# Performance work log

Measured on AMD Instinct MI355X. Metric: run time of the kernel, lower is better.

Reference implementation:

```python
import jax, jax.numpy as jnp
import numpy as np


def setup_inputs() -> dict:
    key = jax.random.key(0)
    k1, k2, k3, k4 = jax.random.split(key, 4)
    B, T, D, U = 64, 2048, 256, 256
    X = jax.random.normal(k1, (B, T, D), dtype=jnp.float32)
    # scale weights ~ Glorot-ish so activations stay in range
    kernel = jax.random.normal(k2, (D, 3 * U), dtype=jnp.float32) / np.sqrt(D)
    recurrent_kernel = jax.random.normal(k3, (U, 3 * U), dtype=jnp.float32) / np.sqrt(U)
    bias = jax.random.normal(k4, (3 * U,), dtype=jnp.float32) * 0.01
    return {"X": X, "kernel": kernel, "recurrent_kernel": recurrent_kernel, "bias": bias}


def reference(X, kernel, recurrent_kernel, bias):
    # X: [B, T, D]; kernel: [D, 3U]; recurrent_kernel: [U, 3U]; bias: [3U]
    U = recurrent_kernel.shape[0]
    B = X.shape[0]
    Uz = recurrent_kernel[:, :U]
    Ur = recurrent_kernel[:, U:2 * U]
    Uh = recurrent_kernel[:, 2 * U:]
    # Precompute input projections for all timesteps in one GEMM (same math
    # as per-step matmul(x, W*) + B*).
    proj = X @ kernel + bias            # [B, T, 3U]
    proj = jnp.swapaxes(proj, 0, 1)     # [T, B, 3U] for scan over time
    xz = proj[:, :, :U]
    xr = proj[:, :, U:2 * U]
    xh = proj[:, :, 2 * U:]

    def step(a, xs):
        tz, tr, th = xs                  # each [B, U]
        z = jax.nn.sigmoid(a @ Uz + tz)
        r = jax.nn.sigmoid(a @ Ur + tr)
        h = jnp.tanh((r * a) @ Uh + th)
        a = z * a + (1.0 - z) * h
        return a, None

    a0 = jnp.zeros((B, U), dtype=X.dtype)
    a_final, _ = jax.lax.scan(step, a0, (xz, xr, xh))
    return a_final  # [B, U]
```

## Files before the change

### kernel.cpp

```cpp
#include <hip/hip_runtime.h>


typedef _Float16 half2_t __attribute__((ext_vector_type(2)));
typedef _Float16 half8_t __attribute__((ext_vector_type(8)));
typedef float    float4_t __attribute__((ext_vector_type(4)));

#define T_LEN 2048
#define B_SZ  64
#define D_IN  256
#define N3    768
#define U_SZ  256

#define H2(v, p) __builtin_shufflevector((v), (v), 2*(p), 2*(p)+1)

__device__ __forceinline__ float fdot2f(half2_t a, half2_t b, float c) {
#if __has_builtin(__builtin_amdgcn_fdot2)
    return __builtin_amdgcn_fdot2(a, b, c, false);
#else
    return c + (float)a[0]*(float)b[0] + (float)a[1]*(float)b[1];
#endif
}

__device__ __forceinline__ float fast_sigmoid(float s) {
    return __builtin_amdgcn_rcpf(1.0f + __builtin_amdgcn_exp2f(-1.44269504f * s));
}
__device__ __forceinline__ float fast_tanh(float s) {
    return 1.0f - 2.0f * __builtin_amdgcn_rcpf(1.0f + __builtin_amdgcn_exp2f(2.88539008f * s));
}

#define GA_LD 264
#define NT_N  16
#define MT_M  2048

__global__ __launch_bounds__(256) void proj_gemm(
    const float* __restrict__ X, const float* __restrict__ W,
    const float* __restrict__ bias, _Float16* __restrict__ proj)
{
    __shared__ __align__(16) _Float16 Ah[64 * GA_LD];
    __shared__ __align__(16) _Float16 Wh[48 * GA_LD];

    unsigned bid = blockIdx.x;
    unsigned idx = bid >> 3;
    unsigned mt  = (bid & 7) * (MT_M / 8) + (idx >> 4);
    unsigned nt  = idx & (NT_N - 1);
    int m0 = mt * 64, n0 = nt * 48;
    int tid = threadIdx.x;

    {
        int r = tid >> 6;
        int k = (tid & 63) * 4;
        #pragma unroll
        for (int i = 0; i < 16; ++i) {
            int row = i * 4 + r;
            float4_t v = *(const float4_t*)(X + (size_t)(m0 + row) * D_IN + k);
            _Float16* p = Ah + row * GA_LD + k;
            p[0] = (_Float16)v.x; p[1] = (_Float16)v.y;
            p[2] = (_Float16)v.z; p[3] = (_Float16)v.w;
        }
    }
    {
        int c  = tid & 63;
        int kk = tid >> 6;
        if (c < 48) {
            #pragma unroll 4
            for (int i = 0; i < 64; ++i) {
                int krow = i * 4 + kk;
                Wh[c * GA_LD + krow] = (_Float16)W[(size_t)krow * N3 + n0 + c];
            }
        }
    }
    __syncthreads();

    int r0 = (tid >> 4) << 2;
    int c  = tid & 15;
    float acc[4][3];
    #pragma unroll
    for (int rr = 0; rr < 4; ++rr)
        #pragma unroll
        for (int cc = 0; cc < 3; ++cc) acc[rr][cc] = 0.0f;

    for (int j = 0; j < 32; ++j) {
        half8_t av[4], wv[3];
        #pragma unroll
        for (int rr = 0; rr < 4; ++rr)
            av[rr] = *(const half8_t*)(Ah + (r0 + rr) * GA_LD + j * 8);
        #pragma unroll
        for (int cc = 0; cc < 3; ++cc)
            wv[cc] = *(const half8_t*)(Wh + (c + 16 * cc) * GA_LD + j * 8);
        #pragma unroll
        for (int rr = 0; rr < 4; ++rr)
            #pragma unroll
            for (int cc = 0; cc < 3; ++cc) {
                acc[rr][cc] = fdot2f(H2(av[rr],0), H2(wv[cc],0), acc[rr][cc]);
                acc[rr][cc] = fdot2f(H2(av[rr],1), H2(wv[cc],1), acc[rr][cc]);
                acc[rr][cc] = fdot2f(H2(av[rr],2), H2(wv[cc],2), acc[rr][cc]);
                acc[rr][cc] = fdot2f(H2(av[rr],3), H2(wv[cc],3), acc[rr][cc]);
            }
    }

    float bv[3];
    #pragma unroll
    for (int cc = 0; cc < 3; ++cc) bv[cc] = bias[n0 + c + 16 * cc];
    #pragma unroll
    for (int rr = 0; rr < 4; ++rr)
        #pragma unroll
        for (int cc = 0; cc < 3; ++cc)
            proj[(size_t)(m0 + r0 + rr) * N3 + (n0 + c + 16 * cc)] =
                (_Float16)(acc[rr][cc] + bv[cc]);
}

__global__ __launch_bounds__(512, 2) void gru_scan(
    const float* __restrict__ RK, const _Float16* __restrict__ proj,
    float* __restrict__ out)
{
    __shared__ __align__(16) _Float16 aH[U_SZ];
    __shared__ __align__(16) _Float16 raH[U_SZ];
    __shared__ float zS[U_SZ];
    __shared__ float aF[U_SZ];

    const int b    = blockIdx.x;
    const int tid  = threadIdx.x;
    const int g    = tid >> 8;
    const int u    = tid & 255;
    const int hcol = tid >> 1;
    const int kh   = tid & 1;

    half2_t wA[128];
    {
        const float* wp = RK + (size_t)(g << 8) + u;
        #pragma unroll
        for (int k2 = 0; k2 < 128; ++k2) {
            half2_t h;
            h[0] = (_Float16)wp[(size_t)(2 * k2)     * N3];
            h[1] = (_Float16)wp[(size_t)(2 * k2 + 1) * N3];
            wA[k2] = h;
        }
    }
    half2_t wB[64];
    {
        const float* wq = RK + (size_t)(kh * 128) * N3 + 512 + hcol;
        #pragma unroll
        for (int k2 = 0; k2 < 64; ++k2) {
            half2_t h;
            h[0] = (_Float16)wq[(size_t)(2 * k2)     * N3];
            h[1] = (_Float16)wq[(size_t)(2 * k2 + 1) * N3];
            wB[k2] = h;
        }
    }

    if (tid < U_SZ) { aF[tid] = 0.0f; aH[tid] = (_Float16)0.0f; }

    const _Float16* px1 = proj + ((size_t)b * T_LEN) * N3 + (g << 8) + u;
    const _Float16* px2 = proj + ((size_t)b * T_LEN) * N3 + 512 + hcol;
    float x1 = (float)px1[0];
    float x2 = (float)px2[0];
    __syncthreads();

    for (int t = 0; t < T_LEN; ++t) {
        const float x1c = x1, x2c = x2;
        if (t + 1 < T_LEN) {
            x1 = (float)px1[(size_t)(t + 1) * N3];
            x2 = (float)px2[(size_t)(t + 1) * N3];
        }

        {
            float a0 = 0.f, a1 = 0.f, a2 = 0.f, a3 = 0.f;
            #pragma unroll
            for (int j = 0; j < 32; ++j) {
                half8_t av = *(const half8_t*)(aH + j * 8);
                a0 = fdot2f(H2(av,0), wA[4*j+0], a0);
                a1 = fdot2f(H2(av,1), wA[4*j+1], a1);
                a2 = fdot2f(H2(av,2), wA[4*j+2], a2);
                a3 = fdot2f(H2(av,3), wA[4*j+3], a3);
            }
            float sig = fast_sigmoid((a0 + a1) + (a2 + a3) + x1c);
            if (g == 0) zS[u]  = sig;
            else        raH[u] = (_Float16)(sig * aF[u]);
        }
        __syncthreads();

        {
            float b0 = 0.f, b1 = 0.f, b2 = 0.f, b3 = 0.f;
            const _Float16* rbase = raH + (kh << 7);
            #pragma unroll
            for (int j = 0; j < 16; ++j) {
                half8_t rv = *(const half8_t*)(rbase + j * 8);
                b0 = fdot2f(H2(rv,0), wB[4*j+0], b0);
                b1 = fdot2f(H2(rv,1), wB[4*j+1], b1);
                b2 = fdot2f(H2(rv,2), wB[4*j+2], b2);
                b3 = fdot2f(H2(rv,3), wB[4*j+3], b3);
            }
            float hs = (b0 + b1) + (b2 + b3);
            hs += __shfl_xor(hs, 1, 64);
            if (kh == 0) {
                float h  = fast_tanh(hs + x2c);
                float z  = zS[hcol];
                float an = z * aF[hcol] + (1.0f - z) * h;
                aF[hcol] = an;
                aH[hcol] = (_Float16)an;
            }
        }
        __syncthreads();
    }

    if (tid < U_SZ) out[(size_t)b * U_SZ + tid] = aF[tid];
}

extern "C" void kernel_launch(void* const* d_in, const int* in_sizes, int n_in,
                              void* d_out, int out_size, void* d_ws, size_t ws_size,
                              hipStream_t stream)
{
    const float* X    = (const float*)d_in[0];
    const float* W    = (const float*)d_in[1];
    const float* RK   = (const float*)d_in[2];
    const float* bias = (const float*)d_in[3];
    _Float16* proj = (_Float16*)d_ws;

    proj_gemm<<<MT_M * NT_N, 256, 0, stream>>>(X, W, bias, proj);
    gru_scan<<<B_SZ, 512, 0, stream>>>(RK, proj, (float*)d_out);
}
```

Before: 3.717 ms.

## Split GRU scan dot products across 1024 threads with shuffle reductions

Doubles the scan block to 1024 threads, so each recurrent-gate column is split over two threads and each candidate column over four, with partial sums combined by warp shuffles. Each thread now does half as many dot-product steps per timestep, which shortens the serial critical path of the recurrence. The cost is extra shuffle and reduction steps, fewer threads doing useful nonlinear work, and a larger block to synchronise at each barrier. Per-thread register weight storage is halved.

```diff
diff --git a/kernel.cpp b/kernel.cpp
--- a/kernel.cpp
+++ b/kernel.cpp
@@ -109,7 +109,7 @@
                 (_Float16)(acc[rr][cc] + bv[cc]);
 }
 
-__global__ __launch_bounds__(512, 2) void gru_scan(
+__global__ __launch_bounds__(1024) void gru_scan(
     const float* __restrict__ RK, const _Float16* __restrict__ proj,
     float* __restrict__ out)
 {
@@ -120,27 +120,27 @@
 
     const int b    = blockIdx.x;
     const int tid  = threadIdx.x;
-    const int g    = tid >> 8;
-    const int u    = tid & 255;
-    const int hcol = tid >> 1;
-    const int kh   = tid & 1;
-
-    half2_t wA[128];
-    {
-        const float* wp = RK + (size_t)(g << 8) + u;
-        #pragma unroll
-        for (int k2 = 0; k2 < 128; ++k2) {
+    const int col1 = tid >> 1;
+    const int kh1  = tid & 1;
+    const int colh = tid >> 2;
+    const int kq   = tid & 3;
+
+    half2_t wA[64];
+    {
+        const float* wp = RK + (size_t)(kh1 * 128) * N3 + col1;
+        #pragma unroll
+        for (int k2 = 0; k2 < 64; ++k2) {
             half2_t h;
             h[0] = (_Float16)wp[(size_t)(2 * k2)     * N3];
             h[1] = (_Float16)wp[(size_t)(2 * k2 + 1) * N3];
             wA[k2] = h;
         }
     }
-    half2_t wB[64];
-    {
-        const float* wq = RK + (size_t)(kh * 128) * N3 + 512 + hcol;
-        #pragma unroll
-        for (int k2 = 0; k2 < 64; ++k2) {
+    half2_t wB[32];
+    {
+        const float* wq = RK + (size_t)(kq * 64) * N3 + 512 + colh;
+        #pragma unroll
+        for (int k2 = 0; k2 < 32; ++k2) {
             half2_t h;
             h[0] = (_Float16)wq[(size_t)(2 * k2)     * N3];
             h[1] = (_Float16)wq[(size_t)(2 * k2 + 1) * N3];
@@ -150,8 +150,8 @@
 
     if (tid < U_SZ) { aF[tid] = 0.0f; aH[tid] = (_Float16)0.0f; }
 
-    const _Float16* px1 = proj + ((size_t)b * T_LEN) * N3 + (g << 8) + u;
-    const _Float16* px2 = proj + ((size_t)b * T_LEN) * N3 + 512 + hcol;
+    const _Float16* px1 = proj + ((size_t)b * T_LEN) * N3 + col1;
+    const _Float16* px2 = proj + ((size_t)b * T_LEN) * N3 + 512 + colh;
     float x1 = (float)px1[0];
     float x2 = (float)px2[0];
     __syncthreads();
@@ -164,40 +164,46 @@
         }
 
         {
-            float a0 = 0.f, a1 = 0.f, a2 = 0.f, a3 = 0.f;
+            float a0 = 0.f, a1 = 0.f;
+            const _Float16* abase = aH + (kh1 << 7);
             #pragma unroll
-            for (int j = 0; j < 32; ++j) {
-                half8_t av = *(const half8_t*)(aH + j * 8);
+            for (int j = 0; j < 16; ++j) {
+                half8_t av = *(const half8_t*)(abase + j * 8);
                 a0 = fdot2f(H2(av,0), wA[4*j+0], a0);
                 a1 = fdot2f(H2(av,1), wA[4*j+1], a1);
-                a2 = fdot2f(H2(av,2), wA[4*j+2], a2);
-                a3 = fdot2f(H2(av,3), wA[4*j+3], a3);
-            }
-            float sig = fast_sigmoid((a0 + a1) + (a2 + a3) + x1c);
-            if (g == 0) zS[u]  = sig;
-            else        raH[u] = (_Float16)(sig * aF[u]);
+                a0 = fdot2f(H2(av,2), wA[4*j+2], a0);
+                a1 = fdot2f(H2(av,3), wA[4*j+3], a1);
+            }
+            float hs = a0 + a1;
+            hs += __shfl_xor(hs, 1, 64);
+            if (kh1 == 0) {
+                float sig = fast_sigmoid(hs + x1c);
+                if (col1 < U_SZ) zS[col1] = sig;
+                else raH[col1 - U_SZ] = (_Float16)(sig * aF[col1 - U_SZ]);
+            }
         }
         __syncthreads();
 
         {
-            float b0 = 0.f, b1 = 0.f, b2 = 0.f, b3 = 0.f;
-            const _Float16* rbase = raH + (kh << 7);
+            float b0 = 0.f, b1 = 0.f;
+            const _Float16* rbase = raH + (kq << 6);
             #pragma unroll
-            for (int j = 0; j < 16; ++j) {
+            for (int j = 0; j < 8; ++j) {
                 half8_t rv = *(const half8_t*)(rbase + j * 8);
                 b0 = fdot2f(H2(rv,0), wB[4*j+0], b0);
                 b1 = fdot2f(H2(rv,1), wB[4*j+1], b1);
-                b2 = fdot2f(H2(rv,2), wB[4*j+2], b2);
-                b3 = fdot2f(H2(rv,3), wB[4*j+3], b3);
-            }
-            float hs = (b0 + b1) + (b2 + b3);
+                b0 = fdot2f(H2(rv,2), wB[4*j+2], b0);
+                b1 = fdot2f(H2(rv,3), wB[4*j+3], b1);
+            }
+            float hs = b0 + b1;
             hs += __shfl_xor(hs, 1, 64);
-            if (kh == 0) {
+            hs += __shfl_xor(hs, 2, 64);
+            if (kq == 0) {
                 float h  = fast_tanh(hs + x2c);
-                float z  = zS[hcol];
-                float an = z * aF[hcol] + (1.0f - z) * h;
-                aF[hcol] = an;
-                aH[hcol] = (_Float16)an;
+                float z  = zS[colh];
+                float an = z * aF[colh] + (1.0f - z) * h;
+                aF[colh] = an;
+                aH[colh] = (_Float16)an;
             }
         }
         __syncthreads();
@@ -217,5 +223,5 @@
     _Float16* proj = (_Float16*)d_ws;
 
     proj_gemm<<<MT_M * NT_N, 256, 0, stream>>>(X, W, bias, proj);
-    gru_scan<<<B_SZ, 512, 0, stream>>>(RK, proj, (float*)d_out);
-}
+    gru_scan<<<B_SZ, 1024, 0, stream>>>(RK, proj, (float*)d_out);
+}
```

Result: slower. 4.887 ms (+31.5%).
